# Kernel optimization log

Hardware: AMD Instinct MI355X
Metric: run time of the kernel (lower is better)

The kernel has to match this reference:

```python
import jax, jax.numpy as jnp
import numpy as np

B, S, D, H, DFF, L, V, LAT = 2, 1800, 128, 8, 512, 6, 16, 1024
DK = D // H


def _pos_encoding():
    # PositionalEncoding buffer, deterministic
    pos = jnp.arange(S, dtype=jnp.float32)[:, None]
    div = jnp.exp(jnp.arange(0, D, 2, dtype=jnp.float32) * (-np.log(10000.0) / D))
    pe = jnp.zeros((S, D), jnp.float32)
    pe = pe.at[:, 0::2].set(jnp.sin(pos * div))
    pe = pe.at[:, 1::2].set(jnp.cos(pos * div))
    return pe  # [S, D]


def _layernorm(x, g, b, eps=1e-5):
    mu = jnp.mean(x, axis=-1, keepdims=True)
    var = jnp.mean((x - mu) ** 2, axis=-1, keepdims=True)
    return (x - mu) / jnp.sqrt(var + eps) * g + b


def _mha(xq, xkv, wq, bq, wk, bk, wv, bv, wo, bo, mask):
    Bq, Sq, _ = xq.shape
    Sk = xkv.shape[1]
    Q = (xq @ wq + bq).reshape(Bq, Sq, H, DK)
    K = (xkv @ wk + bk).reshape(Bq, Sk, H, DK)
    Vv = (xkv @ wv + bv).reshape(Bq, Sk, H, DK)
    scores = jnp.einsum('bqhd,bkhd->bhqk', Q, K) / np.sqrt(DK)
    if mask is not None:
        # faithful to source: masked_fill(mask==0, -1e9) keeps only j>i
        scores = jnp.where(mask, scores, -1e9)
    attn = jax.nn.softmax(scores, axis=-1)
    out = jnp.einsum('bhqk,bkhd->bqhd', attn, Vv).reshape(Bq, Sq, D)
    return out @ wo + bo


def setup_inputs():
    key = jax.random.key(0)
    ks = iter(jax.random.split(key, 40))

    def w(shape, fan_in):
        return (jax.random.normal(next(ks), shape, jnp.float32) / np.sqrt(fan_in))

    inp = {
        'latent': jax.random.normal(next(ks), (B, LAT), jnp.float32),
        'lp_w1': w((LAT, 2 * D), LAT), 'lp_b1': jnp.zeros((2 * D,), jnp.float32),
        'lp_w2': w((2 * D, D * S), 2 * D), 'lp_b2': jnp.zeros((D * S,), jnp.float32),
        'out_w': w((D, V), D), 'out_b': jnp.zeros((V,), jnp.float32),
    }
    for pfx in ('sa', 'ca'):
        for nm in ('q', 'k', 'v', 'o'):
            inp[f'{pfx}_w{nm}'] = w((L, D, D), D)
            inp[f'{pfx}_b{nm}'] = jnp.zeros((L, D), jnp.float32)
    inp['ff_w1'] = w((L, D, DFF), D)
    inp['ff_b1'] = jnp.zeros((L, DFF), jnp.float32)
    inp['ff_w2'] = w((L, DFF, D), DFF)
    inp['ff_b2'] = jnp.zeros((L, D), jnp.float32)
    for i in (1, 2, 3):
        inp[f'ln{i}_g'] = jnp.ones((L, D), jnp.float32)
        inp[f'ln{i}_b'] = jnp.zeros((L, D), jnp.float32)
    return inp


def reference(latent, lp_w1, lp_b1, lp_w2, lp_b2,
              sa_wq, sa_bq, sa_wk, sa_bk, sa_wv, sa_bv, sa_wo, sa_bo,
              ca_wq, ca_bq, ca_wk, ca_bk, ca_wv, ca_bv, ca_wo, ca_bo,
              ff_w1, ff_b1, ff_w2, ff_b2,
              ln1_g, ln1_b, ln2_g, ln2_b, ln3_g, ln3_b,
              out_w, out_b):
    # latent projection -> [B, S, D]
    h = jax.nn.relu(latent @ lp_w1 + lp_b1)
    dec = (h @ lp_w2 + lp_b2).reshape(B, S, D)
    dec = dec + _pos_encoding()[None, :, :]
    # source bug reproduced: only strictly-upper-triangle positions attend
    tgt_mask = jnp.triu(jnp.ones((S, S), bool), 1)
    enc = dec
    x = dec
    for i in range(L):
        a = _mha(x, x, sa_wq[i], sa_bq[i], sa_wk[i], sa_bk[i],
                 sa_wv[i], sa_bv[i], sa_wo[i], sa_bo[i], tgt_mask)
        x = _layernorm(x + a, ln1_g[i], ln1_b[i])
        c = _mha(x, enc, ca_wq[i], ca_bq[i], ca_wk[i], ca_bk[i],
                 ca_wv[i], ca_bv[i], ca_wo[i], ca_bo[i], None)
        x = _layernorm(x + c, ln2_g[i], ln2_b[i])
        f = jax.nn.relu(x @ ff_w1[i] + ff_b1[i]) @ ff_w2[i] + ff_b2[i]
        x = _layernorm(x + f, ln3_g[i], ln3_b[i])
    return x @ out_w + out_b  # [B, S, V]
```

## Files before the change

### kernel.cpp

```cpp
#include <hip/hip_runtime.h>
#include <hip/hip_bf16.h>
#include <math.h>

#define Bn   2
#define Sn   1800
#define Dn   128
#define Hn   8
#define DKn  16
#define DFFn 512
#define Ln   6
#define Vn   16
#define LATn 1024
#define BSn  3600
#define SDn  230400
#define NQT  57
#define VTJ  1824
#define MPAD 3712

typedef __attribute__((ext_vector_type(8))) short short8;
typedef __attribute__((ext_vector_type(16))) float f32x16;
typedef unsigned int u32;
typedef unsigned short u16;

#define ROWMAP(r, hi) (((r) & 3) + 8 * ((r) >> 2) + 4 * (hi))
#define GPERM(sl) (((sl) & 3) + (((sl) & 4) << 1) + (((sl) & 8) >> 1) + ((sl) & 16))

__device__ inline u32 cvtpk_bf16(float a, float b) {
    u32 r;
    asm("v_cvt_pk_bf16_f32 %0, %1, %2" : "=v"(r) : "v"(a), "v"(b));
    return r;
}

__device__ inline u16 f2bf(float f) {
    union { float f; u32 u; } x; x.f = f;
    u32 r = (x.u + 0x7FFFu + ((x.u >> 16) & 1u)) >> 16;
    return (u16)r;
}

__device__ inline float bf2f(u16 v) {
    union { u32 u; float f; } x; x.u = ((u32)v) << 16;
    return x.f;
}

__global__ __launch_bounds__(256) void wconv8_kernel(
    const float* __restrict__ s0, const float* __restrict__ s1,
    const float* __restrict__ s2, const float* __restrict__ s3,
    const float* __restrict__ s4, const float* __restrict__ s5,
    const float* __restrict__ s6, const float* __restrict__ s7,
    u16* __restrict__ d0, u16* __restrict__ d1, u16* __restrict__ d2,
    u16* __restrict__ d3, u16* __restrict__ d4, u16* __restrict__ d5,
    u16* __restrict__ d6, u16* __restrict__ d7)
{
    const int z = blockIdx.z;
    const float* src = (z == 0) ? s0 : (z == 1) ? s1 : (z == 2) ? s2 : (z == 3) ? s3
                     : (z == 4) ? s4 : (z == 5) ? s5 : (z == 6) ? s6 : s7;
    u16* dst = (z == 0) ? d0 : (z == 1) ? d1 : (z == 2) ? d2 : (z == 3) ? d3
             : (z == 4) ? d4 : (z == 5) ? d5 : (z == 6) ? d6 : d7;
    const int id = blockIdx.x * 256 + threadIdx.x;
    const int l = id >> 14, rem = id & 16383;
    const int n = rem >> 7, k = rem & 127;
    dst[id] = f2bf(src[l * 16384 + k * 128 + n]);
}

__global__ __launch_bounds__(256) void wconvg_kernel(
    const float* __restrict__ src, u16* __restrict__ dst, int logK, int logN)
{
    const int id = blockIdx.x * 256 + threadIdx.x;
    const int kn = 1 << (logK + logN);
    const int l = id >> (logK + logN);
    const int rem = id & (kn - 1);
    const int n = rem >> logK, k = rem & ((1 << logK) - 1);
    dst[id] = f2bf(src[(size_t)l * kn + (k << logN) + n]);
}

__global__ __launch_bounds__(256) void zvt_kernel(u16* __restrict__ Vt)
{
    const int id = blockIdx.x * 256 + threadIdx.x;
    const int row = id >> 5, pos = id & 31;
    Vt[(size_t)row * VTJ + 1792 + pos] = 0;
}

__global__ __launch_bounds__(256) void lat_h_kernel(
    const float* __restrict__ latent, const float* __restrict__ w1,
    const float* __restrict__ b1, float* __restrict__ h)
{
    __shared__ float ls[LATn];
    const int b = blockIdx.x;
    const int t = threadIdx.x;
    for (int k = t; k < LATn; k += 256) ls[k] = latent[b * LATn + k];
    __syncthreads();
    float acc = 0.f;
    #pragma unroll 8
    for (int k = 0; k < LATn; ++k) acc = fmaf(ls[k], w1[(size_t)k * 256 + t], acc);
    h[b * 256 + t] = fmaxf(acc + b1[t], 0.f);
}

__global__ __launch_bounds__(256) void dec_kernel(
    const float* __restrict__ h, const float* __restrict__ w2,
    const float* __restrict__ b2, float* __restrict__ x,
    u16* __restrict__ xb, u16* __restrict__ encb)
{
    __shared__ float hs[512];
    const int t = threadIdx.x;
    hs[t] = h[t];
    hs[256 + t] = h[256 + t];
    __syncthreads();
    const int j = blockIdx.x * 256 + t;
    float a0 = 0.f, a1 = 0.f;
    #pragma unroll 8
    for (int k = 0; k < 256; ++k) {
        float w = w2[(size_t)k * SDn + j];
        a0 = fmaf(hs[k], w, a0);
        a1 = fmaf(hs[256 + k], w, a1);
    }
    const int s = j >> 7, d = j & 127;
    const int i2 = d >> 1;
    const float freq = __expf(-(float)(2 * i2) * (9.210340371976184f / 128.f));
    const float ang = (float)s * freq;
    const float pe = (d & 1) ? cosf(ang) : sinf(ang);
    const float bias = b2[j] + pe;
    const float v0 = a0 + bias;
    const float v1 = a1 + bias;
    x[j] = v0;
    x[SDn + j] = v1;
    xb[j] = f2bf(v0);    xb[SDn + j] = f2bf(v1);
    encb[j] = f2bf(v0);  encb[SDn + j] = f2bf(v1);
}

__global__ __launch_bounds__(256) void mm_qkv_kernel(
    const u16* __restrict__ Aq, const u16* __restrict__ Akv,
    const u16* __restrict__ Wq, const u16* __restrict__ Wk, const u16* __restrict__ Wv,
    const float* __restrict__ bq, const float* __restrict__ bk, const float* __restrict__ bv,
    u16* __restrict__ Qb, u16* __restrict__ Kb, u16* __restrict__ Vt)
{
    const int z = blockIdx.z;
    const u16* A = (z == 0) ? Aq : Akv;
    const u16* W = (z == 0) ? Wq : (z == 1) ? Wk : Wv;
    const float* Bi = (z == 0) ? bq : (z == 1) ? bk : bv;

    const int w = threadIdx.x >> 6;
    const int lane = threadIdx.x & 63;
    const int ql = lane & 31, hi = lane >> 5;
    const int m0 = blockIdx.x * 64 + (w & 1) * 32;
    const int nh = (w >> 1) * 64;

    f32x16 acc0 = (f32x16)0.0f, acc1 = (f32x16)0.0f;
    const size_t arow = (size_t)(m0 + ql) * 128;

    #pragma unroll
    for (int kk = 0; kk < 8; ++kk) {
        const short8 a = *(const short8*)(A + arow + kk * 16 + 8 * hi);
        const short8 b0 = *(const short8*)(W + (size_t)(nh + ql) * 128 + kk * 16 + 8 * hi);
        const short8 b1 = *(const short8*)(W + (size_t)(nh + 32 + ql) * 128 + kk * 16 + 8 * hi);
        acc0 = __builtin_amdgcn_mfma_f32_32x32x16_bf16(a, b0, acc0, 0, 0, 0);
        acc1 = __builtin_amdgcn_mfma_f32_32x32x16_bf16(a, b1, acc1, 0, 0, 0);
    }

    #pragma unroll
    for (int j = 0; j < 2; ++j) {
        const int n = nh + j * 32 + ql;
        const float bv_ = Bi[n];
        const int h = n >> 4, d = n & 15;
        #pragma unroll
        for (int r = 0; r < 16; ++r) {
            const int m = m0 + ROWMAP(r, hi);
            if (m >= BSn) continue;
            float v = (j ? acc1[r] : acc0[r]) + bv_;
            const int bq_ = (m >= Sn) ? 1 : 0;
            const int s = m - bq_ * Sn;
            const int bh = bq_ * 8 + h;
            if (z == 0) {
                Qb[((size_t)bh * Sn + s) * 16 + d] = f2bf(v * 0.25f);
            } else if (z == 1) {
                Kb[((size_t)bh * Sn + s) * 16 + d] = f2bf(v);
            } else {
                const int jt = s >> 5, sl = s & 31;
                Vt[((size_t)bh * 16 + d) * VTJ + jt * 32 + GPERM(sl)] = f2bf(v);
            }
        }
    }
}

template <int KS>
__global__ __launch_bounds__(256) void mm_oln_kernel(
    const u16* __restrict__ A, const u16* __restrict__ Wt,
    const float* __restrict__ Bi, const float* __restrict__ xres,
    const float* __restrict__ g, const float* __restrict__ bb,
    float* __restrict__ X, u16* __restrict__ XB)
{
    __shared__ float ls[32 * 132];
    __shared__ float mus[32], invs[32];

    const int t = threadIdx.x;
    const int w = t >> 6;
    const int lane = t & 63;
    const int ql = lane & 31, hi = lane >> 5;
    const int K = KS * 16;
    const int nh = w * 32;
    const int m0 = blockIdx.x * 32;

    f32x16 acc = (f32x16)0.0f;
    const size_t arow = (size_t)(m0 + ql) * K;

    #pragma unroll
    for (int kk = 0; kk < KS; ++kk) {
        const short8 a = *(const short8*)(A + arow + kk * 16 + 8 * hi);
        const short8 b0 = *(const short8*)(Wt + (size_t)(nh + ql) * K + kk * 16 + 8 * hi);
        acc = __builtin_amdgcn_mfma_f32_32x32x16_bf16(a, b0, acc, 0, 0, 0);
    }

    const int n = nh + ql;
    const float bv_ = Bi[n];
    #pragma unroll
    for (int r = 0; r < 16; ++r) {
        const int row = ROWMAP(r, hi);
        const int gm = m0 + row;
        float v = acc[r] + bv_;
        if (gm < BSn) v += xres[(size_t)gm * 128 + n];
        ls[row * 132 + n] = v;
    }
    __syncthreads();

    {
        const int row = t >> 3, q = t & 7;
        float s1 = 0.f, s2 = 0.f;
        const float* lr = &ls[row * 132 + q * 16];
        #pragma unroll
        for (int c = 0; c < 16; c += 4) {
            const float4 v = *(const float4*)&lr[c];
            s1 += v.x + v.y + v.z + v.w;
            s2 += v.x * v.x + v.y * v.y + v.z * v.z + v.w * v.w;
        }
        s1 += __shfl_xor(s1, 1); s2 += __shfl_xor(s2, 1);
        s1 += __shfl_xor(s1, 2); s2 += __shfl_xor(s2, 2);
        s1 += __shfl_xor(s1, 4); s2 += __shfl_xor(s2, 4);
        const float mu = s1 * (1.f / 128.f);
        const float var = s2 * (1.f / 128.f) - mu * mu;
        if (q == 0) { mus[row] = mu; invs[row] = rsqrtf(var + 1e-5f); }
    }
    __syncthreads();

    #pragma unroll
    for (int it = 0; it < 4; ++it) {
        const int idx = it * 256 + t;
        const int row = idx >> 5, cg = (idx & 31) * 4;
        const int gm = m0 + row;
        if (gm >= BSn) continue;
        const float4 v = *(const float4*)&ls[row * 132 + cg];
        const float mu = mus[row], inv = invs[row];
        const float4 gv = *(const float4*)&g[cg];
        const float4 bv2 = *(const float4*)&bb[cg];
        float4 y;
        y.x = (v.x - mu) * inv * gv.x + bv2.x;
        y.y = (v.y - mu) * inv * gv.y + bv2.y;
        y.z = (v.z - mu) * inv * gv.z + bv2.z;
        y.w = (v.w - mu) * inv * gv.w + bv2.w;
        *(float4*)&X[(size_t)gm * 128 + cg] = y;
        uint2 u;
        u.x = cvtpk_bf16(y.x, y.y);
        u.y = cvtpk_bf16(y.z, y.w);
        *(uint2*)&XB[(size_t)gm * 128 + cg] = u;
    }
}

__global__ __launch_bounds__(256) void mm_ff1_kernel(
    const u16* __restrict__ A, const u16* __restrict__ Wt,
    const float* __restrict__ Bi, u16* __restrict__ Hb)
{
    const int t = threadIdx.x;
    const int w = t >> 6;
    const int lane = t & 63;
    const int ql = lane & 31, hi = lane >> 5;
    const int m0 = blockIdx.x * 64 + (w & 1) * 32;
    const int n0 = blockIdx.y * 128 + (w >> 1) * 64;

    f32x16 acc0 = (f32x16)0.0f, acc1 = (f32x16)0.0f;
    const size_t arow = (size_t)(m0 + ql) * 128;

    #pragma unroll
    for (int kk = 0; kk < 8; ++kk) {
        const short8 a = *(const short8*)(A + arow + kk * 16 + 8 * hi);
        const short8 b0 = *(const short8*)(Wt + (size_t)(n0 + ql) * 128 + kk * 16 + 8 * hi);
        const short8 b1 = *(const short8*)(Wt + (size_t)(n0 + 32 + ql) * 128 + kk * 16 + 8 * hi);
        acc0 = __builtin_amdgcn_mfma_f32_32x32x16_bf16(a, b0, acc0, 0, 0, 0);
        acc1 = __builtin_amdgcn_mfma_f32_32x32x16_bf16(a, b1, acc1, 0, 0, 0);
    }

    #pragma unroll
    for (int j = 0; j < 2; ++j) {
        const int n = n0 + j * 32 + ql;
        const float bv_ = Bi[n];
        #pragma unroll
        for (int r = 0; r < 16; ++r) {
            const int m = m0 + ROWMAP(r, hi);
            const float v = fmaxf((j ? acc1[r] : acc0[r]) + bv_, 0.f);
            Hb[(size_t)m * 512 + n] = f2bf(v);
        }
    }
}

template <int MASK>
__global__ __launch_bounds__(256) void flash_mfma(
    const u16* __restrict__ Qb, const u16* __restrict__ Kb,
    const u16* __restrict__ Vt, u16* __restrict__ Ob)
{
    __shared__ float mrg[4][64][10];

    const int wid = threadIdx.x >> 6;
    const int lane = threadIdx.x & 63;
    const int bh = blockIdx.y;
    const int b = bh >> 3, h = bh & 7;

    if (MASK && blockIdx.x == NQT) {
        const int d = threadIdx.x & 15, part = threadIdx.x >> 4;
        const u16* row = Vt + ((size_t)bh * 16 + d) * VTJ;
        float s = 0.f;
        for (int j = part; j < VTJ; j += 16) s += bf2f(row[j]);
        ((float*)mrg)[part * 16 + d] = s;
        __syncthreads();
        if (threadIdx.x < 16) {
            float tot = 0.f;
            #pragma unroll
            for (int p = 0; p < 16; ++p) tot += ((float*)mrg)[p * 16 + threadIdx.x];
            Ob[((size_t)(b * Sn + (Sn - 1))) * 128 + h * 16 + threadIdx.x] =
                f2bf(tot * (1.f / (float)Sn));
        }
        return;
    }

    const int ql = lane & 31, hi = lane >> 5;
    const int qt = blockIdx.x;
    const int qrow = qt * 32 + ql;
    const int qr = (qrow < Sn) ? qrow : (Sn - 1);
    const short8 qf = *(const short8*)(Qb + ((size_t)bh * Sn + qr) * 16 + 8 * hi);
    const u16* kbase = Kb + (size_t)bh * Sn * 16;
    const u16* vbase = Vt + ((size_t)bh * 16 + (ql & 15)) * VTJ;

    f32x16 acc = (f32x16)0.0f;
    float m = -INFINITY, lsum = 0.f;

    int jt = (MASK ? qt : 0) + wid;
    short8 kf = (short8)0, va = (short8)0, vb2 = (short8)0;
    if (jt < NQT) {
        int krow = jt * 32 + ql; if (krow >= Sn) krow = Sn - 1;
        kf  = *(const short8*)(kbase + (size_t)krow * 16 + 8 * hi);
        va  = *(const short8*)(vbase + jt * 32 + 8 * hi);
        vb2 = *(const short8*)(vbase + jt * 32 + 16 + 8 * hi);
    }

    for (; jt < NQT; jt += 4) {
        short8 kn = kf, van = va, vbn = vb2;
        if (jt + 4 < NQT) {
            int nrow = (jt + 4) * 32 + ql; if (nrow >= Sn) nrow = Sn - 1;
            kn  = *(const short8*)(kbase + (size_t)nrow * 16 + 8 * hi);
            van = *(const short8*)(vbase + (jt + 4) * 32 + 8 * hi);
            vbn = *(const short8*)(vbase + (jt + 4) * 32 + 16 + 8 * hi);
        }

        const f32x16 sc = __builtin_amdgcn_mfma_f32_32x32x16_bf16(kf, qf, (f32x16)0.0f, 0, 0, 0);

        float sv[16];
        #pragma unroll
        for (int r = 0; r < 16; ++r) sv[r] = sc[r];

        if (MASK && jt == qt) {
            #pragma unroll
            for (int r = 0; r < 16; ++r)
                if (!(ROWMAP(r, hi) > ql)) sv[r] = -1e9f;
        }
        if (jt == NQT - 1) {
            #pragma unroll
            for (int r = 0; r < 16; ++r)
                if (1792 + ROWMAP(r, hi) >= Sn) sv[r] = -1e30f;
        }

        float tmax = sv[0];
        #pragma unroll
        for (int r = 1; r < 16; ++r) tmax = fmaxf(tmax, sv[r]);
        tmax = fmaxf(tmax, __shfl_xor(tmax, 32));
        const float mnew = fmaxf(m, tmax);
        const float corr = __expf(m - mnew);
        m = mnew;
        lsum *= corr;
        #pragma unroll
        for (int r = 0; r < 16; ++r) acc[r] *= corr;

        float p[16];
        float ps = 0.f;
        #pragma unroll
        for (int r = 0; r < 16; ++r) { p[r] = __expf(sv[r] - mnew); ps += p[r]; }
        lsum += ps;

        union { u32 u[4]; short8 s; } B0c, B1c;
        B0c.u[0] = cvtpk_bf16(p[0],  p[1]);  B0c.u[1] = cvtpk_bf16(p[2],  p[3]);
        B0c.u[2] = cvtpk_bf16(p[4],  p[5]);  B0c.u[3] = cvtpk_bf16(p[6],  p[7]);
        B1c.u[0] = cvtpk_bf16(p[8],  p[9]);  B1c.u[1] = cvtpk_bf16(p[10], p[11]);
        B1c.u[2] = cvtpk_bf16(p[12], p[13]); B1c.u[3] = cvtpk_bf16(p[14], p[15]);

        acc = __builtin_amdgcn_mfma_f32_32x32x16_bf16(va,  B0c.s, acc, 0, 0, 0);
        acc = __builtin_amdgcn_mfma_f32_32x32x16_bf16(vb2, B1c.s, acc, 0, 0, 0);

        kf = kn; va = van; vb2 = vbn;
    }

    mrg[wid][lane][0] = m;
    mrg[wid][lane][1] = lsum;
    #pragma unroll
    for (int r = 0; r < 8; ++r) mrg[wid][lane][2 + r] = acc[r];
    __syncthreads();

    if (wid == 0) {
        float mstar = mrg[0][lane][0];
        #pragma unroll
        for (int w2 = 1; w2 < 4; ++w2) mstar = fmaxf(mstar, mrg[w2][lane][0]);
        float lt = 0.f;
        float accf[8] = {};
        #pragma unroll
        for (int w2 = 0; w2 < 4; ++w2) {
            const float sc2 = __expf(mrg[w2][lane][0] - mstar);
            lt += mrg[w2][lane][1] * sc2;
            #pragma unroll
            for (int r = 0; r < 8; ++r) accf[r] = fmaf(mrg[w2][lane][2 + r], sc2, accf[r]);
        }
        const float ltot = lt + __shfl_xor(lt, 32);
        const float inv = 1.f / ltot;
        if (qrow < Sn && !(MASK && qrow == Sn - 1)) {
            u16* op = Ob + ((size_t)(b * Sn + qrow)) * 128 + h * 16;
            uint2 u0, u1;
            u0.x = cvtpk_bf16(accf[0] * inv, accf[1] * inv);
            u0.y = cvtpk_bf16(accf[2] * inv, accf[3] * inv);
            u1.x = cvtpk_bf16(accf[4] * inv, accf[5] * inv);
            u1.y = cvtpk_bf16(accf[6] * inv, accf[7] * inv);
            *(uint2*)(op + 4 * hi) = u0;
            *(uint2*)(op + 8 + 4 * hi) = u1;
        }
    }
}

__global__ __launch_bounds__(256) void out_kernel(
    const float* __restrict__ X, const float* __restrict__ W,
    const float* __restrict__ bb, float* __restrict__ out)
{
    const int t = threadIdx.x;
    const int n = t & 15;
    const int r = blockIdx.x * 16 + (t >> 4);
    if (r >= BSn) return;
    float acc = 0.f;
    #pragma unroll 8
    for (int k = 0; k < 128; ++k)
        acc = fmaf(X[(size_t)r * 128 + k], W[k * 16 + n], acc);
    out[(size_t)r * 16 + n] = acc + bb[n];
}

extern "C" void kernel_launch(void* const* d_in, const int* in_sizes, int n_in,
                              void* d_out, int out_size, void* d_ws, size_t ws_size,
                              hipStream_t stream)
{
    const float* latent = (const float*)d_in[0];
    const float* lp_w1  = (const float*)d_in[1];
    const float* lp_b1  = (const float*)d_in[2];
    const float* lp_w2  = (const float*)d_in[3];
    const float* lp_b2  = (const float*)d_in[4];
    const float* out_w  = (const float*)d_in[5];
    const float* out_b  = (const float*)d_in[6];
    const float* sa_wq = (const float*)d_in[7];  const float* sa_bq = (const float*)d_in[8];
    const float* sa_wk = (const float*)d_in[9];  const float* sa_bk = (const float*)d_in[10];
    const float* sa_wv = (const float*)d_in[11]; const float* sa_bv = (const float*)d_in[12];
    const float* sa_wo = (const float*)d_in[13]; const float* sa_bo = (const float*)d_in[14];
    const float* ca_wq = (const float*)d_in[15]; const float* ca_bq = (const float*)d_in[16];
    const float* ca_wk = (const float*)d_in[17]; const float* ca_bk = (const float*)d_in[18];
    const float* ca_wv = (const float*)d_in[19]; const float* ca_bv = (const float*)d_in[20];
    const float* ca_wo = (const float*)d_in[21]; const float* ca_bo = (const float*)d_in[22];
    const float* ff_w1 = (const float*)d_in[23]; const float* ff_b1 = (const float*)d_in[24];
    const float* ff_w2 = (const float*)d_in[25]; const float* ff_b2 = (const float*)d_in[26];
    const float* ln1g = (const float*)d_in[27]; const float* ln1b = (const float*)d_in[28];
    const float* ln2g = (const float*)d_in[29]; const float* ln2b = (const float*)d_in[30];
    const float* ln3g = (const float*)d_in[31]; const float* ln3b = (const float*)d_in[32];

    float* ws = (float*)d_ws;
    float* x    = ws;
    float* hlat = ws + 460800;
    u16* xb   = (u16*)(ws + 461312);
    u16* encb = (u16*)(ws + 698880);
    u16* ob   = (u16*)(ws + 936448);
    u16* hb   = (u16*)(ws + 1174016);
    u16* Qb   = (u16*)(ws + 2124288);
    u16* Kb   = (u16*)(ws + 2354688);
    u16* Vt   = (u16*)(ws + 2585088);
    u16* wt_saq = (u16*)(ws + 2818560);
    u16* wt_sak = wt_saq + 6 * 16384;
    u16* wt_sav = wt_sak + 6 * 16384;
    u16* wt_sao = wt_sav + 6 * 16384;
    u16* wt_caq = wt_sao + 6 * 16384;
    u16* wt_cak = wt_caq + 6 * 16384;
    u16* wt_cav = wt_cak + 6 * 16384;
    u16* wt_cao = wt_cav + 6 * 16384;
    u16* wt1  = (u16*)(ws + 3211776);
    u16* wt2  = (u16*)(ws + 3408384);

    wconv8_kernel<<<dim3(384, 1, 8), dim3(256), 0, stream>>>(
        sa_wq, sa_wk, sa_wv, sa_wo, ca_wq, ca_wk, ca_wv, ca_wo,
        wt_saq, wt_sak, wt_sav, wt_sao, wt_caq, wt_cak, wt_cav, wt_cao);
    wconvg_kernel<<<dim3(1536), dim3(256), 0, stream>>>(ff_w1, wt1, 7, 9);
    wconvg_kernel<<<dim3(1536), dim3(256), 0, stream>>>(ff_w2, wt2, 9, 7);
    zvt_kernel<<<dim3(32), dim3(256), 0, stream>>>(Vt);

    lat_h_kernel<<<dim3(2), dim3(256), 0, stream>>>(latent, lp_w1, lp_b1, hlat);
    dec_kernel<<<dim3(900), dim3(256), 0, stream>>>(hlat, lp_w2, lp_b2, x, xb, encb);

    const dim3 thr(256);
    const dim3 gQKV(57, 1, 3), gFF1(57, 4);
    const dim3 gFm(NQT + 1, 16), gFc(NQT, 16);

    for (int i = 0; i < Ln; ++i) {
        const size_t wOff = (size_t)i * 16384;
        const size_t bOff = (size_t)i * 128;
        const size_t fOff = (size_t)i * 65536;
        const size_t f1b  = (size_t)i * 512;

        mm_qkv_kernel<<<gQKV, thr, 0, stream>>>(
            xb, xb, wt_saq + wOff, wt_sak + wOff, wt_sav + wOff,
            sa_bq + bOff, sa_bk + bOff, sa_bv + bOff, Qb, Kb, Vt);
        flash_mfma<1><<<gFm, thr, 0, stream>>>(Qb, Kb, Vt, ob);
        mm_oln_kernel<8><<<dim3(114), thr, 0, stream>>>(
            ob, wt_sao + wOff, sa_bo + bOff, x, ln1g + bOff, ln1b + bOff, x, xb);

        mm_qkv_kernel<<<gQKV, thr, 0, stream>>>(
            xb, encb, wt_caq + wOff, wt_cak + wOff, wt_cav + wOff,
            ca_bq + bOff, ca_bk + bOff, ca_bv + bOff, Qb, Kb, Vt);
        flash_mfma<0><<<gFc, thr, 0, stream>>>(Qb, Kb, Vt, ob);
        mm_oln_kernel<8><<<dim3(114), thr, 0, stream>>>(
            ob, wt_cao + wOff, ca_bo + bOff, x, ln2g + bOff, ln2b + bOff, x, xb);

        mm_ff1_kernel<<<gFF1, thr, 0, stream>>>(xb, wt1 + fOff, ff_b1 + f1b, hb);
        mm_oln_kernel<32><<<dim3(114), thr, 0, stream>>>(
            hb, wt2 + fOff, ff_b2 + bOff, x, ln3g + bOff, ln3b + bOff, x, xb);
    }

    out_kernel<<<dim3(225), dim3(256), 0, stream>>>(x, out_w, out_b, (float*)d_out);
}
```

Measured before the change: 715.4 us.

## Fuse out-proj+LayerNorm with next QKV projection and whole FFN per row tile

Merges the attention output projection, residual and LayerNorm with the following QKV projection in one kernel. The whole FFN (cross-attention out-proj, LN2, FF1, FF2, LN3), plus the next layer's self-attention QKV, runs in a single kernel, with intermediates kept in shared memory. This cuts kernel launches per layer from 8 to 4 and removes global round trips for xb and the hidden activations hb. The trade-off is only 113 blocks with serialized GEMM stages per block, and larger shared memory use, which may lower parallelism and occupancy.

```diff
diff --git a/kernel.cpp b/kernel.cpp
--- a/kernel.cpp
+++ b/kernel.cpp
@@ -181,71 +181,72 @@
     }
 }
 
-template <int KS>
-__global__ __launch_bounds__(256) void mm_oln_kernel(
-    const u16* __restrict__ A, const u16* __restrict__ Wt,
-    const float* __restrict__ Bi, const float* __restrict__ xres,
+__device__ inline void ln_stats(const float* ls, float* mus, float* invs, int t)
+{
+    const int row = t >> 3, q = t & 7;
+    float s1 = 0.f, s2 = 0.f;
+    const float* lr = &ls[row * 132 + q * 16];
+    #pragma unroll
+    for (int c = 0; c < 16; c += 4) {
+        const float4 v = *(const float4*)&lr[c];
+        s1 += v.x + v.y + v.z + v.w;
+        s2 += v.x * v.x + v.y * v.y + v.z * v.z + v.w * v.w;
+    }
+    s1 += __shfl_xor(s1, 1); s2 += __shfl_xor(s2, 1);
+    s1 += __shfl_xor(s1, 2); s2 += __shfl_xor(s2, 2);
+    s1 += __shfl_xor(s1, 4); s2 += __shfl_xor(s2, 4);
+    const float mu = s1 * (1.f / 128.f);
+    const float var = s2 * (1.f / 128.f) - mu * mu;
+    if (q == 0) { mus[row] = mu; invs[row] = rsqrtf(var + 1e-5f); }
+}
+
+__global__ __launch_bounds__(256) void fuse_oln_qkv_kernel(
+    const u16* __restrict__ A, const u16* __restrict__ Wo,
+    const float* __restrict__ bo,
     const float* __restrict__ g, const float* __restrict__ bb,
-    float* __restrict__ X, u16* __restrict__ XB)
+    float* __restrict__ X, const u16* __restrict__ Enc,
+    const u16* __restrict__ Wq, const u16* __restrict__ Wk, const u16* __restrict__ Wv,
+    const float* __restrict__ bq, const float* __restrict__ bk, const float* __restrict__ bv,
+    u16* __restrict__ Qb, u16* __restrict__ Kb, u16* __restrict__ Vt)
 {
     __shared__ float ls[32 * 132];
     __shared__ float mus[32], invs[32];
+    __shared__ alignas(16) u16 ybuf[32][136];
 
     const int t = threadIdx.x;
-    const int w = t >> 6;
-    const int lane = t & 63;
+    const int w = t >> 6, lane = t & 63;
     const int ql = lane & 31, hi = lane >> 5;
-    const int K = KS * 16;
-    const int nh = w * 32;
     const int m0 = blockIdx.x * 32;
 
-    f32x16 acc = (f32x16)0.0f;
-    const size_t arow = (size_t)(m0 + ql) * K;
-
-    #pragma unroll
-    for (int kk = 0; kk < KS; ++kk) {
-        const short8 a = *(const short8*)(A + arow + kk * 16 + 8 * hi);
-        const short8 b0 = *(const short8*)(Wt + (size_t)(nh + ql) * K + kk * 16 + 8 * hi);
-        acc = __builtin_amdgcn_mfma_f32_32x32x16_bf16(a, b0, acc, 0, 0, 0);
-    }
-
-    const int n = nh + ql;
-    const float bv_ = Bi[n];
-    #pragma unroll
-    for (int r = 0; r < 16; ++r) {
-        const int row = ROWMAP(r, hi);
-        const int gm = m0 + row;
-        float v = acc[r] + bv_;
-        if (gm < BSn) v += xres[(size_t)gm * 128 + n];
-        ls[row * 132 + n] = v;
-    }
-    __syncthreads();
-
     {
-        const int row = t >> 3, q = t & 7;
-        float s1 = 0.f, s2 = 0.f;
-        const float* lr = &ls[row * 132 + q * 16];
-        #pragma unroll
-        for (int c = 0; c < 16; c += 4) {
-            const float4 v = *(const float4*)&lr[c];
-            s1 += v.x + v.y + v.z + v.w;
-            s2 += v.x * v.x + v.y * v.y + v.z * v.z + v.w * v.w;
-        }
-        s1 += __shfl_xor(s1, 1); s2 += __shfl_xor(s2, 1);
-        s1 += __shfl_xor(s1, 2); s2 += __shfl_xor(s2, 2);
-        s1 += __shfl_xor(s1, 4); s2 += __shfl_xor(s2, 4);
-        const float mu = s1 * (1.f / 128.f);
-        const float var = s2 * (1.f / 128.f) - mu * mu;
-        if (q == 0) { mus[row] = mu; invs[row] = rsqrtf(var + 1e-5f); }
-    }
-    __syncthreads();
-
+        f32x16 acc = (f32x16)0.0f;
+        const size_t arow = (size_t)(m0 + ql) * 128;
+        const int nh = w * 32;
+        #pragma unroll
+        for (int kk = 0; kk < 8; ++kk) {
+            const short8 a = *(const short8*)(A + arow + kk * 16 + 8 * hi);
+            const short8 b0 = *(const short8*)(Wo + (size_t)(nh + ql) * 128 + kk * 16 + 8 * hi);
+            acc = __builtin_amdgcn_mfma_f32_32x32x16_bf16(a, b0, acc, 0, 0, 0);
+        }
+        const int n = nh + ql;
+        const float bv_ = bo[n];
+        #pragma unroll
+        for (int r = 0; r < 16; ++r) {
+            const int row = ROWMAP(r, hi);
+            const int gm = m0 + row;
+            float v = acc[r] + bv_;
+            if (gm < BSn) v += X[(size_t)gm * 128 + n];
+            ls[row * 132 + n] = v;
+        }
+    }
+    __syncthreads();
+    ln_stats(ls, mus, invs, t);
+    __syncthreads();
     #pragma unroll
     for (int it = 0; it < 4; ++it) {
         const int idx = it * 256 + t;
         const int row = idx >> 5, cg = (idx & 31) * 4;
         const int gm = m0 + row;
-        if (gm >= BSn) continue;
         const float4 v = *(const float4*)&ls[row * 132 + cg];
         const float mu = mus[row], inv = invs[row];
         const float4 gv = *(const float4*)&g[cg];
@@ -255,46 +256,204 @@
         y.y = (v.y - mu) * inv * gv.y + bv2.y;
         y.z = (v.z - mu) * inv * gv.z + bv2.z;
         y.w = (v.w - mu) * inv * gv.w + bv2.w;
-        *(float4*)&X[(size_t)gm * 128 + cg] = y;
+        if (gm < BSn) *(float4*)&X[(size_t)gm * 128 + cg] = y;
         uint2 u;
         u.x = cvtpk_bf16(y.x, y.y);
         u.y = cvtpk_bf16(y.z, y.w);
-        *(uint2*)&XB[(size_t)gm * 128 + cg] = u;
-    }
-}
-
-__global__ __launch_bounds__(256) void mm_ff1_kernel(
-    const u16* __restrict__ A, const u16* __restrict__ Wt,
-    const float* __restrict__ Bi, u16* __restrict__ Hb)
-{
-    const int t = threadIdx.x;
-    const int w = t >> 6;
-    const int lane = t & 63;
-    const int ql = lane & 31, hi = lane >> 5;
-    const int m0 = blockIdx.x * 64 + (w & 1) * 32;
-    const int n0 = blockIdx.y * 128 + (w >> 1) * 64;
-
-    f32x16 acc0 = (f32x16)0.0f, acc1 = (f32x16)0.0f;
-    const size_t arow = (size_t)(m0 + ql) * 128;
-
-    #pragma unroll
-    for (int kk = 0; kk < 8; ++kk) {
-        const short8 a = *(const short8*)(A + arow + kk * 16 + 8 * hi);
-        const short8 b0 = *(const short8*)(Wt + (size_t)(n0 + ql) * 128 + kk * 16 + 8 * hi);
-        const short8 b1 = *(const short8*)(Wt + (size_t)(n0 + 32 + ql) * 128 + kk * 16 + 8 * hi);
-        acc0 = __builtin_amdgcn_mfma_f32_32x32x16_bf16(a, b0, acc0, 0, 0, 0);
-        acc1 = __builtin_amdgcn_mfma_f32_32x32x16_bf16(a, b1, acc1, 0, 0, 0);
-    }
-
-    #pragma unroll
-    for (int j = 0; j < 2; ++j) {
-        const int n = n0 + j * 32 + ql;
+        *(uint2*)&ybuf[row][cg] = u;
+    }
+    __syncthreads();
+
+    #pragma unroll
+    for (int z = 0; z < 3; ++z) {
+        const u16* W = (z == 0) ? Wq : (z == 1) ? Wk : Wv;
+        const float* Bi = (z == 0) ? bq : (z == 1) ? bk : bv;
+        f32x16 acc = (f32x16)0.0f;
+        const int nh = w * 32;
+        #pragma unroll
+        for (int kk = 0; kk < 8; ++kk) {
+            short8 a;
+            if (z == 0) a = *(const short8*)&ybuf[ql][kk * 16 + 8 * hi];
+            else        a = *(const short8*)(Enc + (size_t)(m0 + ql) * 128 + kk * 16 + 8 * hi);
+            const short8 b0 = *(const short8*)(W + (size_t)(nh + ql) * 128 + kk * 16 + 8 * hi);
+            acc = __builtin_amdgcn_mfma_f32_32x32x16_bf16(a, b0, acc, 0, 0, 0);
+        }
+        const int n = nh + ql;
         const float bv_ = Bi[n];
+        const int h = n >> 4, d = n & 15;
         #pragma unroll
         for (int r = 0; r < 16; ++r) {
             const int m = m0 + ROWMAP(r, hi);
-            const float v = fmaxf((j ? acc1[r] : acc0[r]) + bv_, 0.f);
-            Hb[(size_t)m * 512 + n] = f2bf(v);
+            if (m >= BSn) continue;
+            float v = acc[r] + bv_;
+            const int bq_ = (m >= Sn) ? 1 : 0;
+            const int s = m - bq_ * Sn;
+            const int bh = bq_ * 8 + h;
+            if (z == 0)      Qb[((size_t)bh * Sn + s) * 16 + d] = f2bf(v * 0.25f);
+            else if (z == 1) Kb[((size_t)bh * Sn + s) * 16 + d] = f2bf(v);
+            else             Vt[((size_t)bh * 16 + d) * VTJ + (s >> 5) * 32 + GPERM(s & 31)] = f2bf(v);
+        }
+    }
+}
+
+template <int WITH_QKV>
+__global__ __launch_bounds__(256) void fuse_ffn_kernel(
+    const u16* __restrict__ A, const u16* __restrict__ Wo,
+    const float* __restrict__ bo,
+    const float* __restrict__ g2, const float* __restrict__ b2ln,
+    const u16* __restrict__ W1, const float* __restrict__ b1,
+    const u16* __restrict__ W2, const float* __restrict__ b2f,
+    const float* __restrict__ g3, const float* __restrict__ b3ln,
+    float* __restrict__ X,
+    const u16* __restrict__ Wq, const u16* __restrict__ Wk, const u16* __restrict__ Wv,
+    const float* __restrict__ bq, const float* __restrict__ bk, const float* __restrict__ bv,
+    u16* __restrict__ Qb, u16* __restrict__ Kb, u16* __restrict__ Vt)
+{
+    __shared__ float ls[32 * 132];
+    __shared__ float mus[32], invs[32];
+    __shared__ alignas(16) u16 ybuf[32][136];
+    __shared__ alignas(16) u16 hbuf[32][536];
+
+    const int t = threadIdx.x;
+    const int w = t >> 6, lane = t & 63;
+    const int ql = lane & 31, hi = lane >> 5;
+    const int m0 = blockIdx.x * 32;
+
+    {
+        f32x16 acc = (f32x16)0.0f;
+        const size_t arow = (size_t)(m0 + ql) * 128;
+        const int nh = w * 32;
+        #pragma unroll
+        for (int kk = 0; kk < 8; ++kk) {
+            const short8 a = *(const short8*)(A + arow + kk * 16 + 8 * hi);
+            const short8 b0 = *(const short8*)(Wo + (size_t)(nh + ql) * 128 + kk * 16 + 8 * hi);
+            acc = __builtin_amdgcn_mfma_f32_32x32x16_bf16(a, b0, acc, 0, 0, 0);
+        }
+        const int n = nh + ql;
+        const float bv_ = bo[n];
+        #pragma unroll
+        for (int r = 0; r < 16; ++r) {
+            const int row = ROWMAP(r, hi);
+            const int gm = m0 + row;
+            float v = acc[r] + bv_;
+            if (gm < BSn) v += X[(size_t)gm * 128 + n];
+            ls[row * 132 + n] = v;
+        }
+    }
+    __syncthreads();
+    ln_stats(ls, mus, invs, t);
+    __syncthreads();
+    #pragma unroll
+    for (int it = 0; it < 4; ++it) {
+        const int idx = it * 256 + t;
+        const int row = idx >> 5, cg = (idx & 31) * 4;
+        const float4 v = *(const float4*)&ls[row * 132 + cg];
+        const float mu = mus[row], inv = invs[row];
+        const float4 gv = *(const float4*)&g2[cg];
+        const float4 bv2 = *(const float4*)&b2ln[cg];
+        float4 y;
+        y.x = (v.x - mu) * inv * gv.x + bv2.x;
+        y.y = (v.y - mu) * inv * gv.y + bv2.y;
+        y.z = (v.z - mu) * inv * gv.z + bv2.z;
+        y.w = (v.w - mu) * inv * gv.w + bv2.w;
+        *(float4*)&ls[row * 132 + cg] = y;
+        uint2 u;
+        u.x = cvtpk_bf16(y.x, y.y);
+        u.y = cvtpk_bf16(y.z, y.w);
+        *(uint2*)&ybuf[row][cg] = u;
+    }
+    __syncthreads();
+
+    #pragma unroll
+    for (int nt = 0; nt < 4; ++nt) {
+        const int n0 = w * 128 + nt * 32;
+        f32x16 acc = (f32x16)0.0f;
+        #pragma unroll
+        for (int kk = 0; kk < 8; ++kk) {
+            const short8 a = *(const short8*)&ybuf[ql][kk * 16 + 8 * hi];
+            const short8 b0 = *(const short8*)(W1 + (size_t)(n0 + ql) * 128 + kk * 16 + 8 * hi);
+            acc = __builtin_amdgcn_mfma_f32_32x32x16_bf16(a, b0, acc, 0, 0, 0);
+        }
+        const int n = n0 + ql;
+        const float bv_ = b1[n];
+        #pragma unroll
+        for (int r = 0; r < 16; ++r) {
+            const int row = ROWMAP(r, hi);
+            hbuf[row][n] = f2bf(fmaxf(acc[r] + bv_, 0.f));
+        }
+    }
+    __syncthreads();
+
+    {
+        f32x16 acc = (f32x16)0.0f;
+        const int nh = w * 32;
+        #pragma unroll
+        for (int kk = 0; kk < 32; ++kk) {
+            const short8 a = *(const short8*)&hbuf[ql][kk * 16 + 8 * hi];
+            const short8 b0 = *(const short8*)(W2 + (size_t)(nh + ql) * 512 + kk * 16 + 8 * hi);
+            acc = __builtin_amdgcn_mfma_f32_32x32x16_bf16(a, b0, acc, 0, 0, 0);
+        }
+        const int n = nh + ql;
+        const float bv_ = b2f[n];
+        #pragma unroll
+        for (int r = 0; r < 16; ++r) {
+            const int row = ROWMAP(r, hi);
+            ls[row * 132 + n] = acc[r] + bv_ + ls[row * 132 + n];
+        }
+    }
+    __syncthreads();
+    ln_stats(ls, mus, invs, t);
+    __syncthreads();
+    #pragma unroll
+    for (int it = 0; it < 4; ++it) {
+        const int idx = it * 256 + t;
+        const int row = idx >> 5, cg = (idx & 31) * 4;
+        const int gm = m0 + row;
+        const float4 v = *(const float4*)&ls[row * 132 + cg];
+        const float mu = mus[row], inv = invs[row];
+        const float4 gv = *(const float4*)&g3[cg];
+        const float4 bv2 = *(const float4*)&b3ln[cg];
+        float4 y;
+        y.x = (v.x - mu) * inv * gv.x + bv2.x;
+        y.y = (v.y - mu) * inv * gv.y + bv2.y;
+        y.z = (v.z - mu) * inv * gv.z + bv2.z;
+        y.w = (v.w - mu) * inv * gv.w + bv2.w;
+        if (gm < BSn) *(float4*)&X[(size_t)gm * 128 + cg] = y;
+        uint2 u;
+        u.x = cvtpk_bf16(y.x, y.y);
+        u.y = cvtpk_bf16(y.z, y.w);
+        *(uint2*)&ybuf[row][cg] = u;
+    }
+
+    if (WITH_QKV) {
+        __syncthreads();
+        #pragma unroll
+        for (int z = 0; z < 3; ++z) {
+            const u16* W = (z == 0) ? Wq : (z == 1) ? Wk : Wv;
+            const float* Bi = (z == 0) ? bq : (z == 1) ? bk : bv;
+            f32x16 acc = (f32x16)0.0f;
+            const int nh = w * 32;
+            #pragma unroll
+            for (int kk = 0; kk < 8; ++kk) {
+                const short8 a = *(const short8*)&ybuf[ql][kk * 16 + 8 * hi];
+                const short8 b0 = *(const short8*)(W + (size_t)(nh + ql) * 128 + kk * 16 + 8 * hi);
+                acc = __builtin_amdgcn_mfma_f32_32x32x16_bf16(a, b0, acc, 0, 0, 0);
+            }
+            const int n = nh + ql;
+            const float bv_ = Bi[n];
+            const int h = n >> 4, d = n & 15;
+            #pragma unroll
+            for (int r = 0; r < 16; ++r) {
+                const int m = m0 + ROWMAP(r, hi);
+                if (m >= BSn) continue;
+                float v = acc[r] + bv_;
+                const int bq_ = (m >= Sn) ? 1 : 0;
+                const int s = m - bq_ * Sn;
+                const int bh = bq_ * 8 + h;
+                if (z == 0)      Qb[((size_t)bh * Sn + s) * 16 + d] = f2bf(v * 0.25f);
+                else if (z == 1) Kb[((size_t)bh * Sn + s) * 16 + d] = f2bf(v);
+                else             Vt[((size_t)bh * 16 + d) * VTJ + (s >> 5) * 32 + GPERM(s & 31)] = f2bf(v);
+            }
         }
     }
 }
@@ -483,7 +642,6 @@
     u16* xb   = (u16*)(ws + 461312);
     u16* encb = (u16*)(ws + 698880);
     u16* ob   = (u16*)(ws + 936448);
-    u16* hb   = (u16*)(ws + 1174016);
     u16* Qb   = (u16*)(ws + 2124288);
     u16* Kb   = (u16*)(ws + 2354688);
     u16* Vt   = (u16*)(ws + 2585088);
@@ -509,32 +667,42 @@
     dec_kernel<<<dim3(900), dim3(256), 0, stream>>>(hlat, lp_w2, lp_b2, x, xb, encb);
 
     const dim3 thr(256);
-    const dim3 gQKV(57, 1, 3), gFF1(57, 4);
-    const dim3 gFm(NQT + 1, 16), gFc(NQT, 16);
+    const dim3 gFm(NQT + 1, 16), gFc(NQT, 16), gFuse(113);
+
+    mm_qkv_kernel<<<dim3(57, 1, 3), thr, 0, stream>>>(
+        xb, xb, wt_saq, wt_sak, wt_sav, sa_bq, sa_bk, sa_bv, Qb, Kb, Vt);
 
     for (int i = 0; i < Ln; ++i) {
         const size_t wOff = (size_t)i * 16384;
         const size_t bOff = (size_t)i * 128;
         const size_t fOff = (size_t)i * 65536;
         const size_t f1b  = (size_t)i * 512;
-
-        mm_qkv_kernel<<<gQKV, thr, 0, stream>>>(
-            xb, xb, wt_saq + wOff, wt_sak + wOff, wt_sav + wOff,
-            sa_bq + bOff, sa_bk + bOff, sa_bv + bOff, Qb, Kb, Vt);
+        const size_t wNxt = (size_t)(i + 1) * 16384;
+        const size_t bNxt = (size_t)(i + 1) * 128;
+
         flash_mfma<1><<<gFm, thr, 0, stream>>>(Qb, Kb, Vt, ob);
-        mm_oln_kernel<8><<<dim3(114), thr, 0, stream>>>(
-            ob, wt_sao + wOff, sa_bo + bOff, x, ln1g + bOff, ln1b + bOff, x, xb);
-
-        mm_qkv_kernel<<<gQKV, thr, 0, stream>>>(
-            xb, encb, wt_caq + wOff, wt_cak + wOff, wt_cav + wOff,
+
+        fuse_oln_qkv_kernel<<<gFuse, thr, 0, stream>>>(
+            ob, wt_sao + wOff, sa_bo + bOff, ln1g + bOff, ln1b + bOff, x, encb,
+            wt_caq + wOff, wt_cak + wOff, wt_cav + wOff,
             ca_bq + bOff, ca_bk + bOff, ca_bv + bOff, Qb, Kb, Vt);
+
         flash_mfma<0><<<gFc, thr, 0, stream>>>(Qb, Kb, Vt, ob);
-        mm_oln_kernel<8><<<dim3(114), thr, 0, stream>>>(
-            ob, wt_cao + wOff, ca_bo + bOff, x, ln2g + bOff, ln2b + bOff, x, xb);
-
-        mm_ff1_kernel<<<gFF1, thr, 0, stream>>>(xb, wt1 + fOff, ff_b1 + f1b, hb);
-        mm_oln_kernel<32><<<dim3(114), thr, 0, stream>>>(
-            hb, wt2 + fOff, ff_b2 + bOff, x, ln3g + bOff, ln3b + bOff, x, xb);
+
+        if (i < Ln - 1) {
+            fuse_ffn_kernel<1><<<gFuse, thr, 0, stream>>>(
+                ob, wt_cao + wOff, ca_bo + bOff, ln2g + bOff, ln2b + bOff,
+                wt1 + fOff, ff_b1 + f1b, wt2 + fOff, ff_b2 + bOff,
+                ln3g + bOff, ln3b + bOff, x,
+                wt_saq + wNxt, wt_sak + wNxt, wt_sav + wNxt,
+                sa_bq + bNxt, sa_bk + bNxt, sa_bv + bNxt, Qb, Kb, Vt);
+        } else {
+            fuse_ffn_kernel<0><<<gFuse, thr, 0, stream>>>(
+                ob, wt_cao + wOff, ca_bo + bOff, ln2g + bOff, ln2b + bOff,
+                wt1 + fOff, ff_b1 + f1b, wt2 + fOff, ff_b2 + bOff,
+                ln3g + bOff, ln3b + bOff, x,
+                wt_saq, wt_sak, wt_sav, sa_bq, sa_bk, sa_bv, Qb, Kb, Vt);
+        }
     }
 
     out_kernel<<<dim3(225), dim3(256), 0, stream>>>(x, out_w, out_b, (float*)d_out);
```

Result: faster. 616.2 us (-13.9%).
